# Kernel optimization log

Hardware: AMD Instinct MI355X
Metric: run time of the kernel (lower is better)

Reference implementation:

```python
import jax, jax.numpy as jnp
import numpy as np

UFEAT_DIM = 512
EFEAT_DIM = 256
BATCH = 64
PNUM_UNIT = 1024
PNUM_ENEMY = 1024


def setup_inputs() -> dict:
    key = jax.random.key(0)
    k1, k2, k3, k4, k5 = jax.random.split(key, 5)
    ufeat = jax.random.normal(k1, (BATCH, PNUM_UNIT, UFEAT_DIM), dtype=jnp.float32)
    efeat = jax.random.normal(k2, (BATCH, PNUM_ENEMY, EFEAT_DIM), dtype=jnp.float32)
    num_enemy = jax.random.randint(k3, (BATCH,), 0, PNUM_ENEMY, dtype=jnp.int64)
    # weight_norm(Linear, dim=None): W = g * v / ||v||_F, g scalar
    v = jax.random.normal(k4, (EFEAT_DIM, UFEAT_DIM), dtype=jnp.float32) * (1.0 / np.sqrt(UFEAT_DIM))
    g = jnp.asarray(jnp.linalg.norm(v), dtype=jnp.float32)  # init g = ||v||
    b = jax.random.normal(k5, (EFEAT_DIM,), dtype=jnp.float32) * 0.01
    return {"ufeat": ufeat, "efeat": efeat, "num_enemy": num_enemy, "v": v, "g": g, "b": b}


def reference(ufeat, efeat, num_enemy, v, g, b):
    # weight-normed linear (dim=None -> Frobenius norm) + ReLU projection
    W = g * v / jnp.linalg.norm(v)                       # [efeat_dim, ufeat_dim]
    proj = jax.nn.relu(ufeat @ W.T + b)                  # [B, U, efeat_dim]
    # batched dot-product scores (fused matmul instead of repeat+mul+sum)
    norm = jnp.float32(np.sqrt(EFEAT_DIM))
    logit = jnp.einsum('bue,bne->bun', proj, efeat) / norm  # [B, U, N]
    # real-enemy mask: mask[b, n] = 1 iff n < num_enemy[b]
    mask = (jnp.arange(PNUM_ENEMY)[None, :] < num_enemy[:, None]).astype(logit.dtype)
    logit = logit - (1.0 - mask)[:, None, :] * 1e9       # masking bias (uniform if all masked)
    prob = jax.nn.softmax(logit, axis=2)
    return prob
```

## Files before the change

kernel.cpp:

```cpp
#include <hip/hip_runtime.h>
#include <hip/hip_bf16.h>

#define UF 512
#define EF 256
#define NB 64
#define NU 1024
#define NEN 1024

typedef __attribute__((ext_vector_type(8))) short short8;
typedef __attribute__((ext_vector_type(4))) float floatx4;

typedef unsigned short ushort_t;

__device__ inline short2 cvt2(float a, float b) {
    __hip_bfloat162 h = __float22bfloat162_rn(make_float2(a, b));
    union { __hip_bfloat162 h; short2 s; } u;
    u.h = h;
    return u.s;
}

__device__ inline short8 cvt8v(floatx4 x, floatx4 y) {
    union { short8 v; short2 s[4]; } u;
    u.s[0] = cvt2(x[0], x[1]);
    u.s[1] = cvt2(x[2], x[3]);
    u.s[2] = cvt2(y[0], y[1]);
    u.s[3] = cvt2(y[2], y[3]);
    return u.v;
}

__device__ inline ushort_t f2bfbits(float f) {
    unsigned u = __float_as_uint(f);
    u += 0x7FFFu + ((u >> 16) & 1u);
    return (ushort_t)(u >> 16);
}

__global__ void knorm(const float* __restrict__ v, float* __restrict__ ws0) {
    int t = blockIdx.x * 256 + threadIdx.x;
    float2 x = ((const float2*)v)[t];
    float s = x.x * x.x + x.y * x.y;
    #pragma unroll
    for (int m = 1; m < 64; m <<= 1) s += __shfl_xor(s, m);
    __shared__ float ls[4];
    int w = threadIdx.x >> 6;
    if ((threadIdx.x & 63) == 0) ls[w] = s;
    __syncthreads();
    if (threadIdx.x == 0) atomicAdd(ws0, ls[0] + ls[1] + ls[2] + ls[3]);
}

__global__ void kconv(const float* __restrict__ v, const float* __restrict__ g,
                      const float* __restrict__ ef, const float* __restrict__ ws0,
                      const int* __restrict__ nen,
                      ushort_t* __restrict__ wsW, ushort_t* __restrict__ wsE) {
    int bid = blockIdx.x;
    if (bid < 128) {
        int t = bid * 256 + threadIdx.x;
        float s = g[0] * rsqrtf(ws0[0]);
        float4 x = ((const float4*)v)[t];
        short2 a = cvt2(x.x * s, x.y * s);
        short2 b = cvt2(x.z * s, x.w * s);
        ushort4 o;
        o.x = (ushort_t)a.x; o.y = (ushort_t)a.y; o.z = (ushort_t)b.x; o.w = (ushort_t)b.y;
        ((ushort4*)wsW)[t] = o;
    } else {
        long t = (long)(bid - 128) * 256 + threadIdx.x;
        int row = (int)(t >> 6);
        int n = row & (NEN - 1);
        int b = row >> 10;
        if (n < nen[b]) {
            float4 x = ((const float4*)ef)[t];
            short2 a = cvt2(x.x, x.y);
            short2 c = cvt2(x.z, x.w);
            ushort4 o;
            o.x = (ushort_t)a.x; o.y = (ushort_t)a.y; o.z = (ushort_t)c.x; o.w = (ushort_t)c.y;
            ((ushort4*)wsE)[t] = o;
        }
    }
}

__launch_bounds__(256, 2)
__global__ void kgemm1(const float* __restrict__ A, const ushort_t* __restrict__ W,
                       const float* __restrict__ bias, ushort_t* __restrict__ P) {
    const int tid = threadIdx.x;
    const int w = tid >> 6, L = tid & 63;
    const int rA = L & 15, q = L >> 4;
    const long mt = (long)blockIdx.x * 64;

    floatx4 acc[4][4];
    #pragma unroll
    for (int m = 0; m < 4; m++)
        #pragma unroll
        for (int n = 0; n < 4; n++) acc[m][n] = (floatx4){0.f, 0.f, 0.f, 0.f};

    const float* ap[4];
    const ushort_t* wp[4];
    #pragma unroll
    for (int m = 0; m < 4; m++) ap[m] = A + (mt + m * 16 + rA) * UF + q * 8;
    #pragma unroll
    for (int n = 0; n < 4; n++) wp[n] = W + (long)(w * 64 + n * 16 + rA) * UF + q * 8;

    #pragma unroll 2
    for (int s = 0; s < 16; s++) {
        const int ko = s * 32;
        short8 af[4];
        #pragma unroll
        for (int m = 0; m < 4; m++) {
            floatx4 x = __builtin_nontemporal_load((const floatx4*)(ap[m] + ko));
            floatx4 y = __builtin_nontemporal_load((const floatx4*)(ap[m] + ko + 4));
            af[m] = cvt8v(x, y);
        }
        short8 bfr[4];
        #pragma unroll
        for (int n = 0; n < 4; n++) bfr[n] = *(const short8*)(wp[n] + ko);
        #pragma unroll
        for (int n = 0; n < 4; n++)
            #pragma unroll
            for (int m = 0; m < 4; m++)
                acc[m][n] = __builtin_amdgcn_mfma_f32_16x16x32_bf16(af[m], bfr[n], acc[m][n], 0, 0, 0);
    }

    #pragma unroll
    for (int n = 0; n < 4; n++) {
        const int col = w * 64 + n * 16 + rA;
        const float bv = bias[col];
        #pragma unroll
        for (int m = 0; m < 4; m++) {
            #pragma unroll
            for (int i = 0; i < 4; i++) {
                float val = acc[m][n][i] + bv;
                val = fmaxf(val, 0.f);
                const long row = mt + m * 16 + q * 4 + i;
                P[row * EF + col] = f2bfbits(val);
            }
        }
    }
}

__launch_bounds__(256, 2)
__global__ void kattn(const ushort_t* __restrict__ P, const ushort_t* __restrict__ E,
                      const int* __restrict__ nen, float* __restrict__ out) {
    const int tid = threadIdx.x;
    const int w = tid >> 6, L = tid & 63;
    const int rA = L & 15, q = L >> 4;
    const int bid = blockIdx.x;
    const int b = bid >> 5;
    const int ut = bid & 31;
    const int ne = nen[b];

    const ushort_t* prow = P + (long)(b * NU + ut * 32 + rA) * EF + q * 8;
    short8 af[2][8];
    #pragma unroll
    for (int t = 0; t < 2; t++)
        #pragma unroll
        for (int s = 0; s < 8; s++)
            af[t][s] = *(const short8*)(prow + t * 16 * EF + s * 32);

    floatx4 acc[2][16];
    #pragma unroll
    for (int t = 0; t < 2; t++)
        #pragma unroll
        for (int ns = 0; ns < 16; ns++) acc[t][ns] = (floatx4){0.f, 0.f, 0.f, 0.f};
    float psum[2][4];
    #pragma unroll
    for (int t = 0; t < 2; t++)
        #pragma unroll
        for (int i = 0; i < 4; i++) psum[t][i] = 0.f;

    const ushort_t* erow = E + (long)(b * NEN + w * 16 + rA) * EF + q * 8;

    #pragma unroll
    for (int ns = 0; ns < 16; ns++) {
        const int col0 = ns * 64 + w * 16;
        if (col0 < ne) {
            const ushort_t* ep = erow + (long)ns * 64 * EF;
            floatx4 c0 = (floatx4){0.f, 0.f, 0.f, 0.f};
            floatx4 c1 = (floatx4){0.f, 0.f, 0.f, 0.f};
            #pragma unroll
            for (int h = 0; h < 2; h++) {
                short8 bf[4];
                #pragma unroll
                for (int s = 0; s < 4; s++) bf[s] = *(const short8*)(ep + (h * 4 + s) * 32);
                #pragma unroll
                for (int s = 0; s < 4; s++) {
                    c0 = __builtin_amdgcn_mfma_f32_16x16x32_bf16(af[0][h * 4 + s], bf[s], c0, 0, 0, 0);
                    c1 = __builtin_amdgcn_mfma_f32_16x16x32_bf16(af[1][h * 4 + s], bf[s], c1, 0, 0, 0);
                }
            }
            const int col = col0 + rA;
            const bool on = col < ne;
            #pragma unroll
            for (int i = 0; i < 4; i++) {
                float e0 = on ? __expf(c0[i] * 0.0625f) : 0.f;
                float e1 = on ? __expf(c1[i] * 0.0625f) : 0.f;
                c0[i] = e0; c1[i] = e1;
                psum[0][i] += e0; psum[1][i] += e1;
            }
            acc[0][ns] = c0;
            acc[1][ns] = c1;
        }
    }

    #pragma unroll
    for (int t = 0; t < 2; t++)
        #pragma unroll
        for (int i = 0; i < 4; i++) {
            float s = psum[t][i];
            s += __shfl_xor(s, 1);
            s += __shfl_xor(s, 2);
            s += __shfl_xor(s, 4);
            s += __shfl_xor(s, 8);
            psum[t][i] = s;
        }
    __shared__ float lsum[4][32];
    if (rA == 0) {
        #pragma unroll
        for (int t = 0; t < 2; t++)
            #pragma unroll
            for (int i = 0; i < 4; i++)
                lsum[w][t * 16 + q * 4 + i] = psum[t][i];
    }
    __syncthreads();

    float inv[2][4];
    #pragma unroll
    for (int t = 0; t < 2; t++)
        #pragma unroll
        for (int i = 0; i < 4; i++) {
            const int r = t * 16 + q * 4 + i;
            const float tot = lsum[0][r] + lsum[1][r] + lsum[2][r] + lsum[3][r];
            inv[t][i] = (ne > 0) ? (1.f / tot) : 0.f;
        }

    const float uni = 1.f / 1024.f;
    float* orow = out + ((long)(b * NU + ut * 32)) * (long)NEN + w * 16;
    #pragma unroll
    for (int ns = 0; ns < 16; ns++) {
        #pragma unroll
        for (int t = 0; t < 2; t++) {
            #pragma unroll
            for (int i = 0; i < 4; i++) {
                const int u = t * 16 + q * 4 + i;
                const float val = (ne == 0) ? uni : acc[t][ns][i] * inv[t][i];
                __builtin_nontemporal_store(val, &orow[(long)u * NEN + ns * 64 + rA]);
            }
        }
    }
}

extern "C" void kernel_launch(void* const* d_in, const int* in_sizes, int n_in,
                              void* d_out, int out_size, void* d_ws, size_t ws_size,
                              hipStream_t stream) {
    (void)in_sizes; (void)n_in; (void)out_size; (void)ws_size;
    const float* ufeat = (const float*)d_in[0];
    const float* efeat = (const float*)d_in[1];
    const int*   nen   = (const int*)d_in[2];
    const float* v     = (const float*)d_in[3];
    const float* g     = (const float*)d_in[4];
    const float* bias  = (const float*)d_in[5];
    float* out = (float*)d_out;

    float*    ws0 = (float*)d_ws;
    ushort_t* wsW = (ushort_t*)((char*)d_ws + 1024);
    ushort_t* wsE = (ushort_t*)((char*)d_ws + (1u << 20));
    ushort_t* wsP = (ushort_t*)((char*)d_ws + (1u << 20) + (32u << 20));

    hipMemsetAsync(d_ws, 0, 256, stream);
    knorm<<<256, 256, 0, stream>>>(v, ws0);
    kconv<<<16512, 256, 0, stream>>>(v, g, efeat, ws0, nen, wsW, wsE);
    kgemm1<<<1024, 256, 0, stream>>>(ufeat, wsW, bias, wsP);
    kattn<<<2048, 256, 0, stream>>>(wsP, wsE, nen, out);
}
```

Before: 594.1 us.

## Fuse efeat bf16 conversion into attention kernel and halve GEMM1 row tile

Removes the separate efeat fp32-to-bf16 conversion pass and its workspace round trip. The attention kernel now loads fp32 efeat directly and converts it in registers before the MFMA. GEMM1 tiles shrink from 64 to 32 rows per block, doubling the grid, and the A loads change from nontemporal to normal. The cost is that each attention block reads twice as many efeat bytes, and efeat is reread across the 32 u-tiles per batch, though it may hit in cache.

```diff
diff --git a/kernel.cpp b/kernel.cpp
--- a/kernel.cpp
+++ b/kernel.cpp
@@ -47,34 +47,16 @@
     if (threadIdx.x == 0) atomicAdd(ws0, ls[0] + ls[1] + ls[2] + ls[3]);
 }
 
-__global__ void kconv(const float* __restrict__ v, const float* __restrict__ g,
-                      const float* __restrict__ ef, const float* __restrict__ ws0,
-                      const int* __restrict__ nen,
-                      ushort_t* __restrict__ wsW, ushort_t* __restrict__ wsE) {
-    int bid = blockIdx.x;
-    if (bid < 128) {
-        int t = bid * 256 + threadIdx.x;
-        float s = g[0] * rsqrtf(ws0[0]);
-        float4 x = ((const float4*)v)[t];
-        short2 a = cvt2(x.x * s, x.y * s);
-        short2 b = cvt2(x.z * s, x.w * s);
-        ushort4 o;
-        o.x = (ushort_t)a.x; o.y = (ushort_t)a.y; o.z = (ushort_t)b.x; o.w = (ushort_t)b.y;
-        ((ushort4*)wsW)[t] = o;
-    } else {
-        long t = (long)(bid - 128) * 256 + threadIdx.x;
-        int row = (int)(t >> 6);
-        int n = row & (NEN - 1);
-        int b = row >> 10;
-        if (n < nen[b]) {
-            float4 x = ((const float4*)ef)[t];
-            short2 a = cvt2(x.x, x.y);
-            short2 c = cvt2(x.z, x.w);
-            ushort4 o;
-            o.x = (ushort_t)a.x; o.y = (ushort_t)a.y; o.z = (ushort_t)c.x; o.w = (ushort_t)c.y;
-            ((ushort4*)wsE)[t] = o;
-        }
-    }
+__global__ void kconvW(const float* __restrict__ v, const float* __restrict__ g,
+                       const float* __restrict__ ws0, ushort_t* __restrict__ wsW) {
+    int t = blockIdx.x * 256 + threadIdx.x;
+    float s = g[0] * rsqrtf(ws0[0]);
+    float4 x = ((const float4*)v)[t];
+    short2 a = cvt2(x.x * s, x.y * s);
+    short2 b = cvt2(x.z * s, x.w * s);
+    ushort4 o;
+    o.x = (ushort_t)a.x; o.y = (ushort_t)a.y; o.z = (ushort_t)b.x; o.w = (ushort_t)b.y;
+    ((ushort4*)wsW)[t] = o;
 }
 
 __launch_bounds__(256, 2)
@@ -83,39 +65,37 @@
     const int tid = threadIdx.x;
     const int w = tid >> 6, L = tid & 63;
     const int rA = L & 15, q = L >> 4;
-    const long mt = (long)blockIdx.x * 64;
-
-    floatx4 acc[4][4];
-    #pragma unroll
-    for (int m = 0; m < 4; m++)
+    const long mt = (long)blockIdx.x * 32;
+
+    floatx4 acc[2][4];
+    #pragma unroll
+    for (int m = 0; m < 2; m++)
         #pragma unroll
         for (int n = 0; n < 4; n++) acc[m][n] = (floatx4){0.f, 0.f, 0.f, 0.f};
 
-    const float* ap[4];
+    const float* a0 = A + (mt + rA) * UF + q * 8;
+    const float* a1 = A + (mt + 16 + rA) * UF + q * 8;
     const ushort_t* wp[4];
     #pragma unroll
-    for (int m = 0; m < 4; m++) ap[m] = A + (mt + m * 16 + rA) * UF + q * 8;
-    #pragma unroll
     for (int n = 0; n < 4; n++) wp[n] = W + (long)(w * 64 + n * 16 + rA) * UF + q * 8;
 
-    #pragma unroll 2
+    #pragma unroll 4
     for (int s = 0; s < 16; s++) {
         const int ko = s * 32;
-        short8 af[4];
-        #pragma unroll
-        for (int m = 0; m < 4; m++) {
-            floatx4 x = __builtin_nontemporal_load((const floatx4*)(ap[m] + ko));
-            floatx4 y = __builtin_nontemporal_load((const floatx4*)(ap[m] + ko + 4));
-            af[m] = cvt8v(x, y);
-        }
+        floatx4 x0 = *(const floatx4*)(a0 + ko);
+        floatx4 y0 = *(const floatx4*)(a0 + ko + 4);
+        floatx4 x1 = *(const floatx4*)(a1 + ko);
+        floatx4 y1 = *(const floatx4*)(a1 + ko + 4);
+        short8 af0 = cvt8v(x0, y0);
+        short8 af1 = cvt8v(x1, y1);
         short8 bfr[4];
         #pragma unroll
         for (int n = 0; n < 4; n++) bfr[n] = *(const short8*)(wp[n] + ko);
         #pragma unroll
-        for (int n = 0; n < 4; n++)
-            #pragma unroll
-            for (int m = 0; m < 4; m++)
-                acc[m][n] = __builtin_amdgcn_mfma_f32_16x16x32_bf16(af[m], bfr[n], acc[m][n], 0, 0, 0);
+        for (int n = 0; n < 4; n++) {
+            acc[0][n] = __builtin_amdgcn_mfma_f32_16x16x32_bf16(af0, bfr[n], acc[0][n], 0, 0, 0);
+            acc[1][n] = __builtin_amdgcn_mfma_f32_16x16x32_bf16(af1, bfr[n], acc[1][n], 0, 0, 0);
+        }
     }
 
     #pragma unroll
@@ -123,7 +103,7 @@
         const int col = w * 64 + n * 16 + rA;
         const float bv = bias[col];
         #pragma unroll
-        for (int m = 0; m < 4; m++) {
+        for (int m = 0; m < 2; m++) {
             #pragma unroll
             for (int i = 0; i < 4; i++) {
                 float val = acc[m][n][i] + bv;
@@ -136,7 +116,7 @@
 }
 
 __launch_bounds__(256, 2)
-__global__ void kattn(const ushort_t* __restrict__ P, const ushort_t* __restrict__ E,
+__global__ void kattn(const ushort_t* __restrict__ P, const float* __restrict__ E,
                       const int* __restrict__ nen, float* __restrict__ out) {
     const int tid = threadIdx.x;
     const int w = tid >> 6, L = tid & 63;
@@ -165,20 +145,25 @@
         #pragma unroll
         for (int i = 0; i < 4; i++) psum[t][i] = 0.f;
 
-    const ushort_t* erow = E + (long)(b * NEN + w * 16 + rA) * EF + q * 8;
+    const float* erow = E + (long)(b * NEN + w * 16 + rA) * EF + q * 8;
 
     #pragma unroll
     for (int ns = 0; ns < 16; ns++) {
         const int col0 = ns * 64 + w * 16;
         if (col0 < ne) {
-            const ushort_t* ep = erow + (long)ns * 64 * EF;
+            const float* ep = erow + (long)ns * 64 * EF;
             floatx4 c0 = (floatx4){0.f, 0.f, 0.f, 0.f};
             floatx4 c1 = (floatx4){0.f, 0.f, 0.f, 0.f};
             #pragma unroll
             for (int h = 0; h < 2; h++) {
                 short8 bf[4];
                 #pragma unroll
-                for (int s = 0; s < 4; s++) bf[s] = *(const short8*)(ep + (h * 4 + s) * 32);
+                for (int s = 0; s < 4; s++) {
+                    const float* pe = ep + (h * 4 + s) * 32;
+                    floatx4 ex = *(const floatx4*)(pe);
+                    floatx4 ey = *(const floatx4*)(pe + 4);
+                    bf[s] = cvt8v(ex, ey);
+                }
                 #pragma unroll
                 for (int s = 0; s < 4; s++) {
                     c0 = __builtin_amdgcn_mfma_f32_16x16x32_bf16(af[0][h * 4 + s], bf[s], c0, 0, 0, 0);
@@ -260,12 +245,11 @@
 
     float*    ws0 = (float*)d_ws;
     ushort_t* wsW = (ushort_t*)((char*)d_ws + 1024);
-    ushort_t* wsE = (ushort_t*)((char*)d_ws + (1u << 20));
-    ushort_t* wsP = (ushort_t*)((char*)d_ws + (1u << 20) + (32u << 20));
+    ushort_t* wsP = (ushort_t*)((char*)d_ws + (1u << 20));
 
     hipMemsetAsync(d_ws, 0, 256, stream);
     knorm<<<256, 256, 0, stream>>>(v, ws0);
-    kconv<<<16512, 256, 0, stream>>>(v, g, efeat, ws0, nen, wsW, wsE);
-    kgemm1<<<1024, 256, 0, stream>>>(ufeat, wsW, bias, wsP);
-    kattn<<<2048, 256, 0, stream>>>(wsP, wsE, nen, out);
-}
+    kconvW<<<128, 256, 0, stream>>>(v, g, ws0, wsW);
+    kgemm1<<<2048, 256, 0, stream>>>(ufeat, wsW, bias, wsP);
+    kattn<<<2048, 256, 0, stream>>>(wsP, efeat, nen, out);
+}
```

Result: slower. 646.1 us (+8.7%).

## Retile gemm1 waves to 2x2 grid and prefetch A fragments one step ahead

Applied to the files above, without the earlier changes.

Each wave now covers 32 rows by 128 columns instead of 64 rows by 64 columns. This halves how often each wave reads and converts the fp32 activation, and doubles the bf16 weight fragments it loads per step. A loads are software-pipelined one k-step ahead and are no longer nontemporal, so global latency can overlap the MFMAs. The cost is more weight traffic per wave and different register pressure, with the same number of accumulators.

```diff
diff --git a/kernel.cpp b/kernel.cpp
--- a/kernel.cpp
+++ b/kernel.cpp
@@ -81,54 +81,59 @@
 __global__ void kgemm1(const float* __restrict__ A, const ushort_t* __restrict__ W,
                        const float* __restrict__ bias, ushort_t* __restrict__ P) {
     const int tid = threadIdx.x;
-    const int w = tid >> 6, L = tid & 63;
+    const int wv = tid >> 6, L = tid & 63;
     const int rA = L & 15, q = L >> 4;
-    const long mt = (long)blockIdx.x * 64;
-
-    floatx4 acc[4][4];
-    #pragma unroll
-    for (int m = 0; m < 4; m++)
-        #pragma unroll
-        for (int n = 0; n < 4; n++) acc[m][n] = (floatx4){0.f, 0.f, 0.f, 0.f};
-
-    const float* ap[4];
-    const ushort_t* wp[4];
-    #pragma unroll
-    for (int m = 0; m < 4; m++) ap[m] = A + (mt + m * 16 + rA) * UF + q * 8;
-    #pragma unroll
-    for (int n = 0; n < 4; n++) wp[n] = W + (long)(w * 64 + n * 16 + rA) * UF + q * 8;
+    const int mh = wv >> 1;
+    const int nh = wv & 1;
+    const long m0 = (long)blockIdx.x * 64 + mh * 32;
+
+    floatx4 acc[2][8];
+    #pragma unroll
+    for (int m = 0; m < 2; m++)
+        #pragma unroll
+        for (int n = 0; n < 8; n++) acc[m][n] = (floatx4){0.f, 0.f, 0.f, 0.f};
+
+    const float* a0 = A + (m0 + rA) * UF + q * 8;
+    const float* a1 = A + (m0 + 16 + rA) * UF + q * 8;
+    const ushort_t* wb = W + (long)(nh * 128 + rA) * UF + q * 8;
+
+    floatx4 x0 = *(const floatx4*)(a0);
+    floatx4 y0 = *(const floatx4*)(a0 + 4);
+    floatx4 x1 = *(const floatx4*)(a1);
+    floatx4 y1 = *(const floatx4*)(a1 + 4);
 
     #pragma unroll 2
     for (int s = 0; s < 16; s++) {
         const int ko = s * 32;
-        short8 af[4];
-        #pragma unroll
-        for (int m = 0; m < 4; m++) {
-            floatx4 x = __builtin_nontemporal_load((const floatx4*)(ap[m] + ko));
-            floatx4 y = __builtin_nontemporal_load((const floatx4*)(ap[m] + ko + 4));
-            af[m] = cvt8v(x, y);
-        }
-        short8 bfr[4];
-        #pragma unroll
-        for (int n = 0; n < 4; n++) bfr[n] = *(const short8*)(wp[n] + ko);
-        #pragma unroll
-        for (int n = 0; n < 4; n++)
-            #pragma unroll
-            for (int m = 0; m < 4; m++)
-                acc[m][n] = __builtin_amdgcn_mfma_f32_16x16x32_bf16(af[m], bfr[n], acc[m][n], 0, 0, 0);
-    }
-
-    #pragma unroll
-    for (int n = 0; n < 4; n++) {
-        const int col = w * 64 + n * 16 + rA;
+        short8 wf[8];
+        #pragma unroll
+        for (int n = 0; n < 8; n++) wf[n] = *(const short8*)(wb + (long)n * 16 * UF + ko);
+        short8 af0 = cvt8v(x0, y0);
+        short8 af1 = cvt8v(x1, y1);
+        if (s < 15) {
+            x0 = *(const floatx4*)(a0 + ko + 32);
+            y0 = *(const floatx4*)(a0 + ko + 36);
+            x1 = *(const floatx4*)(a1 + ko + 32);
+            y1 = *(const floatx4*)(a1 + ko + 36);
+        }
+        #pragma unroll
+        for (int n = 0; n < 8; n++) {
+            acc[0][n] = __builtin_amdgcn_mfma_f32_16x16x32_bf16(af0, wf[n], acc[0][n], 0, 0, 0);
+            acc[1][n] = __builtin_amdgcn_mfma_f32_16x16x32_bf16(af1, wf[n], acc[1][n], 0, 0, 0);
+        }
+    }
+
+    #pragma unroll
+    for (int n = 0; n < 8; n++) {
+        const int col = nh * 128 + n * 16 + rA;
         const float bv = bias[col];
         #pragma unroll
-        for (int m = 0; m < 4; m++) {
+        for (int m = 0; m < 2; m++) {
             #pragma unroll
             for (int i = 0; i < 4; i++) {
                 float val = acc[m][n][i] + bv;
                 val = fmaxf(val, 0.f);
-                const long row = mt + m * 16 + q * 4 + i;
+                const long row = m0 + m * 16 + q * 4 + i;
                 P[row * EF + col] = f2bfbits(val);
             }
         }
```

Measured after the change: 575.1 us. -3.2%, faster.
